# Performance work log

Hardware: AMD Instinct MI355X
Metric: run time of the kernel (lower is better)

Reference implementation:

```python
import jax, jax.numpy as jnp
import numpy as np
from jax import lax

ROI = 7          # roi_size
STRIDE = 16      # stride_prod
MH = MW = 24     # max crop height/width (fixed-size dynamic_slice window)


def setup_inputs() -> dict:
    key = jax.random.key(0)
    ks = jax.random.split(key, 12)
    N, C, Hf, Wf = 128, 512, 38, 38
    x = jax.random.normal(ks[0], (N, C, Hf, Wf), dtype=jnp.float32)
    # region_projs rows are (r, c, w, h): crop is x[:, c:c+h, r:r+w]
    r = jax.random.randint(ks[1], (N,), 0, 15)
    c = jax.random.randint(ks[2], (N,), 0, 15)
    w = jax.random.randint(ks[3], (N,), 4, MW + 1)
    h = jax.random.randint(ks[4], (N,), 4, MH + 1)
    region_projs = jnp.stack([r, c, w, h], axis=1).astype(jnp.int32)
    W1 = jax.random.normal(ks[5], (ROI * ROI * C, 4096), dtype=jnp.float32) * 0.01
    b1 = jnp.zeros((4096,), dtype=jnp.float32)
    W2 = jax.random.normal(ks[6], (4096, 4096), dtype=jnp.float32) * 0.01
    b2 = jnp.zeros((4096,), dtype=jnp.float32)
    Wcls = jax.random.normal(ks[7], (4096, 21), dtype=jnp.float32) * 0.01
    Wbox = jax.random.normal(ks[8], (4096, 80), dtype=jnp.float32) * 0.001
    return {"x": x, "region_projs": region_projs, "W1": W1, "b1": b1,
            "W2": W2, "b2": b2, "Wcls": Wcls, "Wbox": Wbox}


def _roi_adaptive_maxpool(crops, w, h):
    """crops: [N,C,MH,MW]; w,h: [N] int (valid extent). AdaptiveMaxPool2d((7,7)) per ROI."""
    ii = jnp.arange(ROI)
    ys = jnp.arange(MH)
    xs = jnp.arange(MW)
    # adaptive pool bin i of length L covers [floor(i*L/7), ceil((i+1)*L/7))
    rstart = (ii[None, :] * h[:, None]) // ROI            # [N,7]
    rend = ((ii[None, :] + 1) * h[:, None] + ROI - 1) // ROI
    cstart = (ii[None, :] * w[:, None]) // ROI
    cend = ((ii[None, :] + 1) * w[:, None] + ROI - 1) // ROI
    rmask = (ys[None, None, :] >= rstart[:, :, None]) & (ys[None, None, :] < rend[:, :, None])  # [N,7,MH]
    cmask = (xs[None, None, :] >= cstart[:, :, None]) & (xs[None, None, :] < cend[:, :, None])  # [N,7,MW]
    neg = jnp.float32(-jnp.inf)
    rows = [jnp.max(jnp.where(rmask[:, i, None, :, None], crops, neg), axis=2) for i in range(ROI)]
    tmp = jnp.stack(rows, axis=2)  # [N,C,7,MW]
    cols = [jnp.max(jnp.where(cmask[:, j, None, None, :], tmp, neg), axis=3) for j in range(ROI)]
    return jnp.stack(cols, axis=3)  # [N,C,7,7]


def reference(x, region_projs, W1, b1, W2, b2, Wcls, Wbox):
    N, C = x.shape[0], x.shape[1]
    # per-ROI crop: x[idx, :, c:c+h, r:r+w]; fixed-size window, bins mask the valid extent
    crops = jax.vmap(
        lambda xi, b: lax.dynamic_slice(xi, (0, b[1], b[0]), (C, MH, MW))
    )(x, region_projs)  # [N,C,MH,MW]
    pooled = _roi_adaptive_maxpool(crops, region_projs[:, 2], region_projs[:, 3])
    flat = pooled.reshape(N, -1)  # [N, 25088]
    # classifier (Dropout in eval mode = identity)
    h1 = jax.nn.relu(flat @ W1 + b1)
    h2 = jax.nn.relu(h1 @ W2 + b2)
    clf_scores = jax.nn.softmax(h2 @ Wcls, axis=1)          # [N,21]
    bbox_targets = h2 @ Wbox                                 # [N,80]
    # bbox_target_to_pred_bbox, vectorized over rois and classes
    bf = region_projs.astype(jnp.float32)
    r, c, w, h = bf[:, 0:1], bf[:, 1:2], bf[:, 2:3], bf[:, 3:4]  # [N,1]
    t = bbox_targets.reshape(N, 20, 4)
    p0 = jnp.ceil((w * t[..., 0] + r) * STRIDE) - 1.0
    p1 = jnp.ceil((h * t[..., 1] + c) * STRIDE) - 1.0
    p2 = jnp.floor(w * jnp.exp(t[..., 2]) * STRIDE) + 1.0
    p3 = jnp.floor(h * jnp.exp(t[..., 3]) * STRIDE) + 1.0
    bbox_pred = jnp.stack([p0, p1, p2, p3], axis=-1).reshape(N, 80)
    bbox_pred = lax.stop_gradient(bbox_pred)  # torch path detaches via math.ceil/floor
    return clf_scores, bbox_pred
```

## Files before the change

kernel.cpp:

```cpp
#include <hip/hip_runtime.h>
#include <hip/hip_bf16.h>
#include <math.h>

#define N_BATCH 128
#define C_CH    512
#define HF      38
#define WF      38
#define K1      25088
#define NH      4096
#define NCLS    21
#define NBOX    80
#define STEPS1  784
#define STEPS2  128

typedef __attribute__((ext_vector_type(8))) short s16x8;
typedef __attribute__((ext_vector_type(4))) float f32x4;

__device__ __forceinline__ unsigned short bf_rne(float x) {
  unsigned u = __float_as_uint(x);
  return (unsigned short)((u + 0x7FFFu + ((u >> 16) & 1u)) >> 16);
}
__device__ __forceinline__ float bf2f(unsigned short b) {
  return __uint_as_float(((unsigned)b) << 16);
}
__device__ __forceinline__ void split3(float x, unsigned short& q0,
                                       unsigned short& q1, unsigned short& q2) {
  q0 = bf_rne(x); float r1 = x - bf2f(q0);
  q1 = bf_rne(r1); float r2 = r1 - bf2f(q1);
  q2 = bf_rne(r2);
}

__device__ __forceinline__ void gload16(const void* g, void* l) {
  __builtin_amdgcn_global_load_lds(
      (const __attribute__((address_space(1))) unsigned int*)g,
      (__attribute__((address_space(3))) unsigned int*)l, 16, 0, 0);
}

__global__ __launch_bounds__(256) void pool_kernel(
    const float* __restrict__ x, const int* __restrict__ rp,
    unsigned short* __restrict__ Asw) {
  const int n = blockIdx.y, cb = blockIdx.x, tid = threadIdx.x;
  const int r = rp[n*4+0], c = rp[n*4+1], w = rp[n*4+2], h = rp[n*4+3];
  __shared__ float tile[8][24][25];
  const int ch = tid >> 5, l32 = tid & 31;
  const float* xc = x + (((size_t)(n*C_CH + cb*8 + ch))*HF + c)*WF + r;
  for (int y = 0; y < h; ++y)
    for (int xx = l32; xx < w; xx += 32)
      tile[ch][y][xx] = xc[y*WF + xx];
  __syncthreads();
  const int mt = n >> 4, mlo = n & 15;
  for (int o = tid; o < 8*49; o += 256) {
    int ch2 = o / 49, ij = o - ch2*49, i = ij / 7, j = ij - i*7;
    int rs = (i*h)/7, re = ((i+1)*h + 6)/7;
    int cs = (j*w)/7, ce = ((j+1)*w + 6)/7;
    float m = -INFINITY;
    for (int y = rs; y < re; ++y)
      for (int xx = cs; xx < ce; ++xx)
        m = fmaxf(m, tile[ch2][y][xx]);
    int k = (cb*8 + ch2)*49 + ij;
    int S = k >> 5, kg = (k >> 3) & 3, e = k & 7;
    size_t base = ((size_t)S*8 + mt)*1536 + (size_t)(kg*16 + mlo)*8 + e;
    unsigned short q0, q1, q2; split3(m, q0, q1, q2);
    Asw[base] = q0; Asw[base + 512] = q1; Asw[base + 1024] = q2;
  }
}

__global__ __launch_bounds__(256, 2) void gemm_v7(
    const unsigned short* __restrict__ Asw, const float* __restrict__ B,
    float* __restrict__ part, const int nsteps) {
  __shared__ float Bsm[4][2][32][64];
  const int tid = threadIdx.x, lane = tid & 63, wv = tid >> 6;
  const int wr = wv >> 1, wc = wv & 1;
  const int nb = blockIdx.x, ks = blockIdx.y;
  const int l15 = lane & 15, lq = lane >> 4;
  const unsigned short* Ag = Asw + (size_t)ks*nsteps*12288 + lane*8;
  const int srow4 = lane >> 4, scol16 = lane & 15;
  const float* Bg = B + ((size_t)ks*nsteps*32 + srow4)*NH
                  + (size_t)nb*128 + wc*64;

  f32x4 acc[4][4];
  #pragma unroll
  for (int i = 0; i < 4; ++i)
    #pragma unroll
    for (int j = 0; j < 4; ++j) acc[i][j] = (f32x4){0.f, 0.f, 0.f, 0.f};

  s16x8 w0[4], w1[4], w2[4];
#define LOADA(slot, g) do { \
    const unsigned short* ap_ = Ag + (size_t)(g)*1536; \
    w0[slot] = *(const s16x8*)ap_; \
    w1[slot] = *(const s16x8*)(ap_ + 512); \
    w2[slot] = *(const s16x8*)(ap_ + 1024); } while (0)

  float* ldsb = &Bsm[wv][0][0][0];
#define STAGEB(s, buf) do { \
    float* dst_ = ldsb + (buf)*2048; \
    _Pragma("unroll") \
    for (int i_ = 0; i_ < 8; ++i_) \
      gload16(Bg + ((size_t)(s)*32 + i_*4)*NH \
                 + ((scol16*4) ^ (8*((i_ >> 1) & 3))), dst_ + i_*256); \
    } while (0)

  STAGEB(0, 0);
  LOADA(0, wr*4 + 0); LOADA(1, wr*4 + 1);
  LOADA(2, wr*4 + 2); LOADA(3, wr*4 + 3);

  for (int s = 0; s < nsteps; ++s) {
    if (s + 1 < nsteps) {
      STAGEB(s + 1, (s + 1) & 1);
      asm volatile("s_waitcnt vmcnt(20)" ::: "memory");
    } else {
      asm volatile("s_waitcnt vmcnt(12)" ::: "memory");
    }
    const float* bb = ldsb + (s & 1)*2048;
    s16x8 bf0[4], bf1[4], bf2[4];
    #pragma unroll
    for (int nt = 0; nt < 4; ++nt) {
      #pragma unroll
      for (int e = 0; e < 8; ++e) {
        float xv = bb[(lq*8 + e)*64 + ((nt*16 + l15) ^ (lq*8))];
        unsigned short q0, q1, q2; split3(xv, q0, q1, q2);
        bf0[nt][e] = (short)q0; bf1[nt][e] = (short)q1; bf2[nt][e] = (short)q2;
      }
    }
    #pragma unroll
    for (int ml = 0; ml < 4; ++ml) {
      const s16x8 a0 = w0[ml], a1 = w1[ml], a2 = w2[ml];
      LOADA(ml, (s + 1)*8 + wr*4 + ml);
      #pragma unroll
      for (int nt = 0; nt < 4; ++nt) {
        f32x4 cc = acc[ml][nt];
        cc = __builtin_amdgcn_mfma_f32_16x16x32_bf16(a0, bf0[nt], cc, 0, 0, 0);
        cc = __builtin_amdgcn_mfma_f32_16x16x32_bf16(a0, bf1[nt], cc, 0, 0, 0);
        cc = __builtin_amdgcn_mfma_f32_16x16x32_bf16(a1, bf0[nt], cc, 0, 0, 0);
        cc = __builtin_amdgcn_mfma_f32_16x16x32_bf16(a0, bf2[nt], cc, 0, 0, 0);
        cc = __builtin_amdgcn_mfma_f32_16x16x32_bf16(a1, bf1[nt], cc, 0, 0, 0);
        cc = __builtin_amdgcn_mfma_f32_16x16x32_bf16(a2, bf0[nt], cc, 0, 0, 0);
        acc[ml][nt] = cc;
      }
    }
  }
#undef LOADA
#undef STAGEB
  float* Pb = part + (size_t)ks*N_BATCH*NH + (size_t)nb*128 + wc*64;
  #pragma unroll
  for (int ml = 0; ml < 4; ++ml)
    #pragma unroll
    for (int nt = 0; nt < 4; ++nt)
      #pragma unroll
      for (int rr = 0; rr < 4; ++rr)
        Pb[(size_t)((wr*4 + ml)*16 + lq*4 + rr)*NH + nt*16 + l15]
            = acc[ml][nt][rr];
}

__global__ __launch_bounds__(256) void reduce_k(
    const float* __restrict__ part, const float* __restrict__ bias,
    unsigned short* __restrict__ AswOut, float* __restrict__ f32out,
    int KS, int mode) {
  const int idx = blockIdx.x*256 + threadIdx.x;
  float4 s = ((const float4*)part)[idx];
  for (int k2 = 1; k2 < KS; ++k2) {
    float4 p = ((const float4*)part)[(size_t)k2*131072 + idx];
    s.x += p.x; s.y += p.y; s.z += p.z; s.w += p.w;
  }
  float4 bv = ((const float4*)bias)[idx & 1023];
  float v[4];
  v[0] = fmaxf(s.x + bv.x, 0.f); v[1] = fmaxf(s.y + bv.y, 0.f);
  v[2] = fmaxf(s.z + bv.z, 0.f); v[3] = fmaxf(s.w + bv.w, 0.f);
  if (mode == 1) {
    float4 o; o.x = v[0]; o.y = v[1]; o.z = v[2]; o.w = v[3];
    ((float4*)f32out)[idx] = o;
  } else {
    int m = idx >> 10, k = (idx & 1023) * 4;
    int S = k >> 5, kg = (k >> 3) & 3, e0 = k & 7;
    size_t base = ((size_t)S*8 + (m >> 4))*1536
                + (size_t)(kg*16 + (m & 15))*8 + e0;
    unsigned short q[3][4];
    #pragma unroll
    for (int e = 0; e < 4; ++e) split3(v[e], q[0][e], q[1][e], q[2][e]);
    #pragma unroll
    for (int p = 0; p < 3; ++p) {
      ushort4 st; st.x=q[p][0]; st.y=q[p][1]; st.z=q[p][2]; st.w=q[p][3];
      *(ushort4*)(AswOut + base + p*512) = st;
    }
  }
}

__global__ __launch_bounds__(256) void head_transpose(
    const float* __restrict__ Wcls, const float* __restrict__ Wbox,
    float* __restrict__ WT) {
  const int c = blockIdx.x;
  const float* src; int stride;
  if (c < NCLS) { src = Wcls + c; stride = NCLS; }
  else          { src = Wbox + (c - NCLS); stride = NBOX; }
  for (int k = threadIdx.x; k < NH; k += 256)
    WT[(size_t)c*NH + k] = src[(size_t)k*stride];
}

__global__ __launch_bounds__(256) void head_dots(
    const float* __restrict__ h2, const float* __restrict__ WT,
    float* __restrict__ hout) {
  const int n = blockIdx.y;
  const int wv = threadIdx.x >> 6, lane = threadIdx.x & 63;
  const int c = blockIdx.x * 4 + wv;
  if (c >= NCLS + NBOX) return;
  const float4* hp = (const float4*)(h2 + (size_t)n*NH);
  const float4* wp = (const float4*)(WT + (size_t)c*NH);
  float s0=0.f, s1=0.f, s2=0.f, s3=0.f;
  #pragma unroll
  for (int it = 0; it < 16; ++it) {
    float4 a = hp[it*64 + lane];
    float4 b = wp[it*64 + lane];
    s0 = fmaf(a.x, b.x, s0); s1 = fmaf(a.y, b.y, s1);
    s2 = fmaf(a.z, b.z, s2); s3 = fmaf(a.w, b.w, s3);
  }
  float v = (s0 + s1) + (s2 + s3);
  #pragma unroll
  for (int m = 32; m >= 1; m >>= 1) v += __shfl_xor(v, m, 64);
  if (lane == 0) hout[n*128 + c] = v;
}

__global__ __launch_bounds__(128) void head_final(
    const float* __restrict__ hout, const int* __restrict__ rp,
    float* __restrict__ out) {
  const int n = blockIdx.x, tid = threadIdx.x;
  __shared__ float logits[NCLS];
  __shared__ float red[2];
  if (tid < NCLS) logits[tid] = hout[n*128 + tid];
  __syncthreads();
  if (tid == 0) {
    float m = logits[0];
    for (int i = 1; i < NCLS; ++i) m = fmaxf(m, logits[i]);
    float s = 0.f;
    for (int i = 0; i < NCLS; ++i) s += expf(logits[i] - m);
    red[0] = m; red[1] = s;
  }
  __syncthreads();
  if (tid < NCLS) {
    out[(size_t)n*NCLS + tid] = expf(logits[tid] - red[0]) / red[1];
  } else if (tid < NCLS + NBOX) {
    const int j = tid - NCLS;
    const float t  = hout[n*128 + tid];
    const float rf = (float)rp[n*4+0];
    const float cf = (float)rp[n*4+1];
    const float wf = (float)rp[n*4+2];
    const float hf = (float)rp[n*4+3];
    float p;
    switch (j & 3) {
      case 0:  p = ceilf (__fmul_rn(__fadd_rn(__fmul_rn(wf, t), rf), 16.f)) - 1.f; break;
      case 1:  p = ceilf (__fmul_rn(__fadd_rn(__fmul_rn(hf, t), cf), 16.f)) - 1.f; break;
      case 2:  p = floorf(__fmul_rn(__fmul_rn(wf, expf(t)), 16.f)) + 1.f; break;
      default: p = floorf(__fmul_rn(__fmul_rn(hf, expf(t)), 16.f)) + 1.f; break;
    }
    out[(size_t)N_BATCH*NCLS + (size_t)n*NBOX + j] = p;
  }
}

extern "C" void kernel_launch(void* const* d_in, const int* in_sizes, int n_in,
                              void* d_out, int out_size, void* d_ws, size_t ws_size,
                              hipStream_t stream) {
  const float* x    = (const float*)d_in[0];
  const int*   rp   = (const int*)  d_in[1];
  const float* W1   = (const float*)d_in[2];
  const float* b1   = (const float*)d_in[3];
  const float* W2   = (const float*)d_in[4];
  const float* b2   = (const float*)d_in[5];
  const float* Wcls = (const float*)d_in[6];
  const float* Wbox = (const float*)d_in[7];
  float* out = (float*)d_out;

  char* wp = (char*)d_ws;
  unsigned short* Asw1 = (unsigned short*)wp; wp += (size_t)STEPS1*24576;
  unsigned short* Asw2 = (unsigned short*)wp; wp += (size_t)STEPS2*24576;
  float* h2f = (float*)wp;            wp += (size_t)N_BATCH*NH*4;
  float* WT  = (float*)wp;            wp += (size_t)(NCLS+NBOX)*NH*4;
  float* hout = (float*)wp;           wp += (size_t)N_BATCH*128*4;
  float* part = (float*)wp;
  const size_t fixed = (size_t)(wp - (char*)d_ws);
  const size_t slab = (size_t)N_BATCH*NH*4;
  int KS1 = 16, KS2 = 16;
  if (fixed + 16*slab > ws_size) { KS1 = 8; KS2 = 8; }

  pool_kernel<<<dim3(64, 128), 256, 0, stream>>>(x, rp, Asw1);
  head_transpose<<<dim3(NCLS + NBOX), 256, 0, stream>>>(Wcls, Wbox, WT);

  gemm_v7<<<dim3(32, KS1), 256, 0, stream>>>(Asw1, W1, part, STEPS1/KS1);
  reduce_k<<<dim3(512), 256, 0, stream>>>(part, b1, Asw2, nullptr, KS1, 0);

  gemm_v7<<<dim3(32, KS2), 256, 0, stream>>>(Asw2, W2, part, STEPS2/KS2);
  reduce_k<<<dim3(512), 256, 0, stream>>>(part, b2, nullptr, h2f, KS2, 1);

  head_dots<<<dim3(26, 128), 256, 0, stream>>>(h2f, WT, hout);
  head_final<<<dim3(128), 128, 0, stream>>>(hout, rp, out);
}
```

Baseline: 299.3 us.

## Interleave B split with MFMA bursts, template GEMM tile width, vectorize pool stores

```diff
diff --git a/kernel.cpp b/kernel.cpp
--- a/kernel.cpp
+++ b/kernel.cpp
@@ -42,13 +42,13 @@
   const int n = blockIdx.y, cb = blockIdx.x, tid = threadIdx.x;
   const int r = rp[n*4+0], c = rp[n*4+1], w = rp[n*4+2], h = rp[n*4+3];
   __shared__ float tile[8][24][25];
+  __shared__ float pout[392];
   const int ch = tid >> 5, l32 = tid & 31;
   const float* xc = x + (((size_t)(n*C_CH + cb*8 + ch))*HF + c)*WF + r;
   for (int y = 0; y < h; ++y)
     for (int xx = l32; xx < w; xx += 32)
       tile[ch][y][xx] = xc[y*WF + xx];
   __syncthreads();
-  const int mt = n >> 4, mlo = n & 15;
   for (int o = tid; o < 8*49; o += 256) {
     int ch2 = o / 49, ij = o - ch2*49, i = ij / 7, j = ij - i*7;
     int rs = (i*h)/7, re = ((i+1)*h + 6)/7;
@@ -57,32 +57,53 @@
     for (int y = rs; y < re; ++y)
       for (int xx = cs; xx < ce; ++xx)
         m = fmaxf(m, tile[ch2][y][xx]);
-    int k = (cb*8 + ch2)*49 + ij;
-    int S = k >> 5, kg = (k >> 3) & 3, e = k & 7;
-    size_t base = ((size_t)S*8 + mt)*1536 + (size_t)(kg*16 + mlo)*8 + e;
-    unsigned short q0, q1, q2; split3(m, q0, q1, q2);
-    Asw[base] = q0; Asw[base + 512] = q1; Asw[base + 1024] = q2;
-  }
-}
-
-__global__ __launch_bounds__(256, 2) void gemm_v7(
+    pout[o] = m;
+  }
+  __syncthreads();
+  if (tid < 49) {
+    const int mt = n >> 4, mlo = n & 15;
+    const int kl0 = tid * 8;
+    const int kg0 = cb*392 + kl0;
+    const int S = kg0 >> 5, kg = (kg0 >> 3) & 3;
+    size_t base = ((size_t)S*8 + mt)*1536 + (size_t)(kg*16 + mlo)*8;
+    unsigned short q[3][8];
+    #pragma unroll
+    for (int e = 0; e < 8; ++e)
+      split3(pout[kl0 + e], q[0][e], q[1][e], q[2][e]);
+    #pragma unroll
+    for (int p = 0; p < 3; ++p) {
+      ushort4 lo; lo.x=q[p][0]; lo.y=q[p][1]; lo.z=q[p][2]; lo.w=q[p][3];
+      ushort4 hi; hi.x=q[p][4]; hi.y=q[p][5]; hi.z=q[p][6]; hi.w=q[p][7];
+      *(ushort4*)(Asw + base + p*512)     = lo;
+      *(ushort4*)(Asw + base + p*512 + 4) = hi;
+    }
+  }
+}
+
+template<int NT, int MINW>
+__global__ __launch_bounds__(256, MINW) void gemm_v10(
     const unsigned short* __restrict__ Asw, const float* __restrict__ B,
     float* __restrict__ part, const int nsteps) {
-  __shared__ float Bsm[4][2][32][64];
+  constexpr int NCOLS = NT * 16;
+  constexpr int SB = 2 * NT;
+  constexpr int LPR = NT * 4;
+  constexpr int RPO = 64 / LPR;
+  __shared__ float Bsm[4][2][32][NCOLS];
   const int tid = threadIdx.x, lane = tid & 63, wv = tid >> 6;
   const int wr = wv >> 1, wc = wv & 1;
   const int nb = blockIdx.x, ks = blockIdx.y;
   const int l15 = lane & 15, lq = lane >> 4;
   const unsigned short* Ag = Asw + (size_t)ks*nsteps*12288 + lane*8;
-  const int srow4 = lane >> 4, scol16 = lane & 15;
-  const float* Bg = B + ((size_t)ks*nsteps*32 + srow4)*NH
-                  + (size_t)nb*128 + wc*64;
-
-  f32x4 acc[4][4];
+  const int srow = lane / LPR, scol = lane % LPR;
+  const float* Bg = B + ((size_t)ks*nsteps*32 + srow)*NH
+                  + (size_t)nb*(2*NCOLS) + wc*NCOLS;
+  float* ldsb = &Bsm[wv][0][0][0];
+
+  f32x4 acc[4][NT];
   #pragma unroll
   for (int i = 0; i < 4; ++i)
     #pragma unroll
-    for (int j = 0; j < 4; ++j) acc[i][j] = (f32x4){0.f, 0.f, 0.f, 0.f};
+    for (int j = 0; j < NT; ++j) acc[i][j] = (f32x4){0.f, 0.f, 0.f, 0.f};
 
   s16x8 w0[4], w1[4], w2[4];
 #define LOADA(slot, g) do { \
@@ -91,14 +112,37 @@
     w1[slot] = *(const s16x8*)(ap_ + 512); \
     w2[slot] = *(const s16x8*)(ap_ + 1024); } while (0)
 
-  float* ldsb = &Bsm[wv][0][0][0];
 #define STAGEB(s, buf) do { \
-    float* dst_ = ldsb + (buf)*2048; \
+    float* dst_ = ldsb + (buf)*(32*NCOLS); \
     _Pragma("unroll") \
-    for (int i_ = 0; i_ < 8; ++i_) \
-      gload16(Bg + ((size_t)(s)*32 + i_*4)*NH \
-                 + ((scol16*4) ^ (8*((i_ >> 1) & 3))), dst_ + i_*256); \
-    } while (0)
+    for (int i_ = 0; i_ < SB; ++i_) { \
+      const int row_ = i_*RPO + srow; \
+      gload16(Bg + ((size_t)(s)*32 + (size_t)i_*RPO)*NH \
+                 + ((scol*4) ^ (8*((row_ >> 3) & 3))), dst_ + i_*256); \
+    } } while (0)
+
+#define SPLITNT(nt, B0, B1, B2) do { \
+    _Pragma("unroll") \
+    for (int e_ = 0; e_ < 8; ++e_) { \
+      float xv_ = bb[(lq*8 + e_)*NCOLS + (((nt)*16 + l15) ^ (lq*8))]; \
+      unsigned short q0_, q1_, q2_; split3(xv_, q0_, q1_, q2_); \
+      B0[e_] = (short)q0_; B1[e_] = (short)q1_; B2[e_] = (short)q2_; \
+    } } while (0)
+
+#define BURST(nt, B0, B1, B2, DO_LOADA) do { \
+    _Pragma("unroll") \
+    for (int ml_ = 0; ml_ < 4; ++ml_) { \
+      const s16x8 a0_ = w0[ml_], a1_ = w1[ml_], a2_ = w2[ml_]; \
+      if (DO_LOADA) LOADA(ml_, (s + 1)*8 + wr*4 + ml_); \
+      f32x4 cc_ = acc[ml_][nt]; \
+      cc_ = __builtin_amdgcn_mfma_f32_16x16x32_bf16(a0_, B0, cc_, 0, 0, 0); \
+      cc_ = __builtin_amdgcn_mfma_f32_16x16x32_bf16(a0_, B1, cc_, 0, 0, 0); \
+      cc_ = __builtin_amdgcn_mfma_f32_16x16x32_bf16(a1_, B0, cc_, 0, 0, 0); \
+      cc_ = __builtin_amdgcn_mfma_f32_16x16x32_bf16(a0_, B2, cc_, 0, 0, 0); \
+      cc_ = __builtin_amdgcn_mfma_f32_16x16x32_bf16(a1_, B1, cc_, 0, 0, 0); \
+      cc_ = __builtin_amdgcn_mfma_f32_16x16x32_bf16(a2_, B0, cc_, 0, 0, 0); \
+      acc[ml_][nt] = cc_; \
+    } } while (0)
 
   STAGEB(0, 0);
   LOADA(0, wr*4 + 0); LOADA(1, wr*4 + 1);
@@ -107,45 +151,37 @@
   for (int s = 0; s < nsteps; ++s) {
     if (s + 1 < nsteps) {
       STAGEB(s + 1, (s + 1) & 1);
-      asm volatile("s_waitcnt vmcnt(20)" ::: "memory");
+      if constexpr (NT == 4) {
+        asm volatile("s_waitcnt vmcnt(8)" ::: "memory");
+      } else {
+        asm volatile("s_waitcnt vmcnt(4)" ::: "memory");
+      }
     } else {
-      asm volatile("s_waitcnt vmcnt(12)" ::: "memory");
-    }
-    const float* bb = ldsb + (s & 1)*2048;
-    s16x8 bf0[4], bf1[4], bf2[4];
-    #pragma unroll
-    for (int nt = 0; nt < 4; ++nt) {
-      #pragma unroll
-      for (int e = 0; e < 8; ++e) {
-        float xv = bb[(lq*8 + e)*64 + ((nt*16 + l15) ^ (lq*8))];
-        unsigned short q0, q1, q2; split3(xv, q0, q1, q2);
-        bf0[nt][e] = (short)q0; bf1[nt][e] = (short)q1; bf2[nt][e] = (short)q2;
-      }
-    }
-    #pragma unroll
-    for (int ml = 0; ml < 4; ++ml) {
-      const s16x8 a0 = w0[ml], a1 = w1[ml], a2 = w2[ml];
-      LOADA(ml, (s + 1)*8 + wr*4 + ml);
-      #pragma unroll
-      for (int nt = 0; nt < 4; ++nt) {
-        f32x4 cc = acc[ml][nt];
-        cc = __builtin_amdgcn_mfma_f32_16x16x32_bf16(a0, bf0[nt], cc, 0, 0, 0);
-        cc = __builtin_amdgcn_mfma_f32_16x16x32_bf16(a0, bf1[nt], cc, 0, 0, 0);
-        cc = __builtin_amdgcn_mfma_f32_16x16x32_bf16(a1, bf0[nt], cc, 0, 0, 0);
-        cc = __builtin_amdgcn_mfma_f32_16x16x32_bf16(a0, bf2[nt], cc, 0, 0, 0);
-        cc = __builtin_amdgcn_mfma_f32_16x16x32_bf16(a1, bf1[nt], cc, 0, 0, 0);
-        cc = __builtin_amdgcn_mfma_f32_16x16x32_bf16(a2, bf0[nt], cc, 0, 0, 0);
-        acc[ml][nt] = cc;
-      }
+      asm volatile("s_waitcnt vmcnt(0)" ::: "memory");
+    }
+    __builtin_amdgcn_sched_barrier(0);
+    const float* bb = ldsb + (s & 1)*(32*NCOLS);
+    s16x8 pA0, pA1, pA2, pB0, pB1, pB2;
+    SPLITNT(0, pA0, pA1, pA2);
+    if constexpr (NT == 4) {
+      SPLITNT(1, pB0, pB1, pB2); BURST(0, pA0, pA1, pA2, false);
+      SPLITNT(2, pA0, pA1, pA2); BURST(1, pB0, pB1, pB2, false);
+      SPLITNT(3, pB0, pB1, pB2); BURST(2, pA0, pA1, pA2, false);
+      BURST(3, pB0, pB1, pB2, true);
+    } else {
+      SPLITNT(1, pB0, pB1, pB2); BURST(0, pA0, pA1, pA2, false);
+      BURST(1, pB0, pB1, pB2, true);
     }
   }
 #undef LOADA
 #undef STAGEB
-  float* Pb = part + (size_t)ks*N_BATCH*NH + (size_t)nb*128 + wc*64;
+#undef SPLITNT
+#undef BURST
+  float* Pb = part + (size_t)ks*N_BATCH*NH + (size_t)nb*(2*NCOLS) + wc*NCOLS;
   #pragma unroll
   for (int ml = 0; ml < 4; ++ml)
     #pragma unroll
-    for (int nt = 0; nt < 4; ++nt)
+    for (int nt = 0; nt < NT; ++nt)
       #pragma unroll
       for (int rr = 0; rr < 4; ++rr)
         Pb[(size_t)((wr*4 + ml)*16 + lq*4 + rr)*NH + nt*16 + l15]
@@ -283,10 +319,10 @@
   pool_kernel<<<dim3(64, 128), 256, 0, stream>>>(x, rp, Asw1);
   head_transpose<<<dim3(NCLS + NBOX), 256, 0, stream>>>(Wcls, Wbox, WT);
 
-  gemm_v7<<<dim3(32, KS1), 256, 0, stream>>>(Asw1, W1, part, STEPS1/KS1);
+  gemm_v10<4, 2><<<dim3(32, KS1), 256, 0, stream>>>(Asw1, W1, part, STEPS1/KS1);
   reduce_k<<<dim3(512), 256, 0, stream>>>(part, b1, Asw2, nullptr, KS1, 0);
 
-  gemm_v7<<<dim3(32, KS2), 256, 0, stream>>>(Asw2, W2, part, STEPS2/KS2);
+  gemm_v10<2, 2><<<dim3(64, KS2), 256, 0, stream>>>(Asw2, W2, part, STEPS2/KS2);
   reduce_k<<<dim3(512), 256, 0, stream>>>(part, b2, nullptr, h2f, KS2, 1);
 
   head_dots<<<dim3(26, 128), 256, 0, stream>>>(h2f, WT, hout);
```

After: 316.1 us. 5.6% more time.
